# Kernel tuning notes

Hardware: AMD Instinct MI355X
Metric: run time of the kernel (lower is better)

## Reference

```python
import jax, jax.numpy as jnp
import numpy as np

# Tree / encoder dims (see shape_source): root + 4 middle + 16 leaves
T_DATA = 100000
T_V = 100
WIN = 2 * T_V - 1          # (T_V-1)*2 + 1 = 199, first MLP in_dim
HID = 256                  # hid_dim
N_MID = 4                  # numel(in_idx_list[0])  (middle-level latents)
N_LEAF = 16                # numel(out_idx_list[-1]) (leaf-level latents)


def setup_inputs() -> dict:
    key = jax.random.key(0)
    ks = jax.random.split(key, 6)
    sc = lambda k, shape, fan: jax.random.normal(k, shape, jnp.float32) * (1.0 / np.sqrt(fan))
    return {
        "V_in": jax.random.normal(ks[0], (T_DATA,), jnp.float32),
        "W1": sc(ks[1], (WIN, HID), WIN),
        "b1": jnp.zeros((HID,), jnp.float32),
        "W2": sc(ks[2], (HID, N_MID), HID),
        "b2": jnp.zeros((N_MID,), jnp.float32),
        # leaf_encoder = MLP(HID, HID, N_LEAF)
        "Wl1": sc(ks[3], (HID, HID), HID),
        "bl1": jnp.zeros((HID,), jnp.float32),
        "Wl2": sc(ks[4], (HID, N_LEAF), HID),
        "bl2": jnp.zeros((N_LEAF,), jnp.float32),
    }


def reference(V_in, W1, b1, W2, b2, Wl1, bl1, Wl2, bl2):
    """Vectorized LVAE_shGLM.Encoder: the original loops over every timestep t,
    slicing pad_V_in[t:t+2*T_V-1] and running MLP.encode chains per step.
    Here all T windows are processed as one batched GEMM chain.
    MLP.encode(x) = (h = relu(x@W1+b1), mu = h@W2+b2)."""
    T = V_in.shape[0]
    pad = jnp.zeros((T + 2 * (T_V - 1),), V_in.dtype).at[T_V - 1:T_V - 1 + T].set(V_in)
    idx = jnp.arange(T)[:, None] + jnp.arange(WIN)[None, :]
    windows = pad[idx]
    # middle encoder (level 0 of the dendritic tree)
    h_mid = jax.nn.relu(windows @ W1 + b1)          # [T, HID]
    mu_mid = h_mid @ W2 + b2                        # [T, N_MID]
    # leaf encoder consumes the middle hidden state
    h_leaf = jax.nn.relu(h_mid @ Wl1 + bl1)         # [T, HID]
    mu_leaf = h_leaf @ Wl2 + bl2                    # [T, N_LEAF]
    # up_mu_array[t] = [middle mus (count 0..N_MID), leaf mus (N_MID..sub_no-1)]
    return jnp.concatenate([mu_mid, mu_leaf], axis=1)  # [T, sub_no-1] = [T, 20]
```

## Files before the change

kernel.cpp:

```cpp
#include <hip/hip_runtime.h>


typedef __bf16 bf16;
typedef __bf16 bf16x8 __attribute__((ext_vector_type(8)));
typedef float  f32x4  __attribute__((ext_vector_type(4)));
typedef float  f32x16 __attribute__((ext_vector_type(16)));

constexpr int T_DATA = 100000;
constexpr int T_V    = 100;
constexpr int WIN    = 199;
constexpr int HID    = 256;
constexpr int BT     = 64;
constexpr int HSTR   = 264;
constexpr int VLEN   = 288;
constexpr int VSTR   = 296;

constexpr int PWL1_OFF = 104 * 512;
constexpr int PW2_OFF  = 232 * 512;
constexpr int PWL2_OFF = 240 * 512;

__global__ void pack_weights(const float* __restrict__ W1, const float* __restrict__ W2,
                             const float* __restrict__ Wl1, const float* __restrict__ Wl2,
                             bf16* __restrict__ ws) {
  const int gid  = blockIdx.x * blockDim.x + threadIdx.x;
  const int lane = gid & 63;
  const int grp  = gid >> 6;
  bf16x8 v;
  if (grp < 104) {
    const int kt = grp >> 3, nt = grp & 7, n = nt * 32 + (lane & 31);
#pragma unroll
    for (int j = 0; j < 8; ++j) {
      const int k = kt * 16 + (lane >> 5) * 8 + j;
      v[j] = (k < WIN) ? (bf16)W1[k * HID + n] : (bf16)0.0f;
    }
  } else if (grp < 232) {
    const int q = grp - 104;
    const int kt = q >> 3, nt = q & 7, n = nt * 32 + (lane & 31);
#pragma unroll
    for (int j = 0; j < 8; ++j) {
      const int k = kt * 16 + (lane >> 5) * 8 + j;
      v[j] = (bf16)Wl1[k * HID + n];
    }
  } else if (grp < 240) {
    const int kt = grp - 232, m = lane & 15;
#pragma unroll
    for (int j = 0; j < 8; ++j) {
      const int k = kt * 32 + (lane >> 4) * 8 + j;
      v[j] = (m < 4) ? (bf16)W2[k * 4 + m] : (bf16)0.0f;
    }
  } else {
    const int kt = grp - 240, m = lane & 15;
#pragma unroll
    for (int j = 0; j < 8; ++j) {
      const int k = kt * 32 + (lane >> 4) * 8 + j;
      v[j] = (bf16)Wl2[k * 16 + m];
    }
  }
  *reinterpret_cast<bf16x8*>(ws + (size_t)gid * 8) = v;
}

__global__ __launch_bounds__(512, 4) void fused_enc(
    const float* __restrict__ V, const float* __restrict__ b1,
    const float* __restrict__ b2, const float* __restrict__ bl1,
    const float* __restrict__ bl2, const bf16* __restrict__ ws,
    float* __restrict__ out) {
  __shared__ bf16 Vdup[8][VSTR];
  __shared__ bf16 hmid[BT * HSTR];
  __shared__ bf16 hleaf[BT * HSTR];

  const int tid  = threadIdx.x;
  const int lane = tid & 63;
  const int w    = tid >> 6;
  const int c5   = lane & 31;
  const int hi   = lane >> 5;
  const int m    = lane & 15;
  const int g    = lane >> 4;
  const long t0  = (long)blockIdx.x * BT;

  for (int c = tid; c < 8 * VLEN; c += 512) {
    const int p = c / VLEN, q = c - p * VLEN;
    const long src = t0 + q + p - (T_V - 1);
    const float v = (src >= 0 && src < T_DATA) ? V[src] : 0.0f;
    Vdup[p][q] = (bf16)v;
  }
  __syncthreads();

  const int p  = lane & 7;
  const int qb = (c5 + hi * 8) - p;
  const bf16* vrow = &Vdup[p][0];

  f32x16 acc0 = {}, acc1 = {};

#pragma unroll
  for (int kt = 0; kt < 13; ++kt) {
    const bf16x8 b  = *reinterpret_cast<const bf16x8*>(
        ws + (size_t)(kt * 8 + w) * 512 + lane * 8);
    const bf16x8 a0 = *reinterpret_cast<const bf16x8*>(vrow + qb + kt * 16);
    const bf16x8 a1 = *reinterpret_cast<const bf16x8*>(vrow + qb + kt * 16 + 32);
    acc0 = __builtin_amdgcn_mfma_f32_32x32x16_bf16(a0, b, acc0, 0, 0, 0);
    acc1 = __builtin_amdgcn_mfma_f32_32x32x16_bf16(a1, b, acc1, 0, 0, 0);
  }

  const int   col = w * 32 + c5;
  const float bb1 = b1[col];
#pragma unroll
  for (int r = 0; r < 16; ++r) {
    const int row = (r & 3) + 8 * (r >> 2) + 4 * hi;
    hmid[row * HSTR + col]        = (bf16)fmaxf(acc0[r] + bb1, 0.0f);
    hmid[(row + 32) * HSTR + col] = (bf16)fmaxf(acc1[r] + bb1, 0.0f);
  }
  __syncthreads();

  acc0 = (f32x16){};
  acc1 = (f32x16){};
#pragma unroll
  for (int kt = 0; kt < 16; ++kt) {
    const bf16x8 b  = *reinterpret_cast<const bf16x8*>(
        ws + PWL1_OFF + (size_t)(kt * 8 + w) * 512 + lane * 8);
    const int koff = kt * 16 + hi * 8;
    const bf16x8 a0 = *reinterpret_cast<const bf16x8*>(&hmid[c5 * HSTR + koff]);
    const bf16x8 a1 = *reinterpret_cast<const bf16x8*>(&hmid[(32 + c5) * HSTR + koff]);
    acc0 = __builtin_amdgcn_mfma_f32_32x32x16_bf16(a0, b, acc0, 0, 0, 0);
    acc1 = __builtin_amdgcn_mfma_f32_32x32x16_bf16(a1, b, acc1, 0, 0, 0);
  }

  const float bbl = bl1[col];
#pragma unroll
  for (int r = 0; r < 16; ++r) {
    const int row = (r & 3) + 8 * (r >> 2) + 4 * hi;
    hleaf[row * HSTR + col]        = (bf16)fmaxf(acc0[r] + bbl, 0.0f);
    hleaf[(row + 32) * HSTR + col] = (bf16)fmaxf(acc1[r] + bbl, 0.0f);
  }
  __syncthreads();

  const bf16* hb   = (w < 4) ? hmid : hleaf;
  const bf16* bwp  = ws + ((w < 4) ? PW2_OFF : PWL2_OFF);
  const int   wr   = w & 3;
  f32x4 mu = {0.f, 0.f, 0.f, 0.f};
#pragma unroll
  for (int kt = 0; kt < 8; ++kt) {
    const bf16x8 a = *reinterpret_cast<const bf16x8*>(
        &hb[(wr * 16 + m) * HSTR + kt * 32 + g * 8]);
    const bf16x8 b = *reinterpret_cast<const bf16x8*>(bwp + (size_t)kt * 512 + lane * 8);
    mu = __builtin_amdgcn_mfma_f32_16x16x32_bf16(a, b, mu, 0, 0, 0);
  }

  if (w < 4) {
    const float b2v = (m < 4) ? b2[m] : 0.0f;
#pragma unroll
    for (int j = 0; j < 4; ++j) {
      const long t = t0 + wr * 16 + g * 4 + j;
      if (t < T_DATA && m < 4) out[t * 20 + m] = mu[j] + b2v;
    }
  } else {
    const float blv = bl2[m];
#pragma unroll
    for (int j = 0; j < 4; ++j) {
      const long t = t0 + wr * 16 + g * 4 + j;
      if (t < T_DATA) out[t * 20 + 4 + m] = mu[j] + blv;
    }
  }
}

extern "C" void kernel_launch(void* const* d_in, const int* in_sizes, int n_in,
                              void* d_out, int out_size, void* d_ws, size_t ws_size,
                              hipStream_t stream) {
  const float* V   = (const float*)d_in[0];
  const float* W1  = (const float*)d_in[1];
  const float* b1  = (const float*)d_in[2];
  const float* W2  = (const float*)d_in[3];
  const float* b2  = (const float*)d_in[4];
  const float* Wl1 = (const float*)d_in[5];
  const float* bl1 = (const float*)d_in[6];
  const float* Wl2 = (const float*)d_in[7];
  const float* bl2 = (const float*)d_in[8];
  bf16* ws = (bf16*)d_ws;
  float* out = (float*)d_out;

  pack_weights<<<62, 256, 0, stream>>>(W1, W2, Wl1, Wl2, ws);

  const int grid = (T_DATA + BT - 1) / BT;
  fused_enc<<<grid, 512, 0, stream>>>(V, b1, b2, bl1, bl2, ws, out);
}
```

Measured before the change: 43.76 us.

## Double row tile to 128 and reuse one shared buffer for both hidden layers

Result: faster. 42.75 us (-2.3%).

```diff
diff --git a/kernel.cpp b/kernel.cpp
--- a/kernel.cpp
+++ b/kernel.cpp
@@ -10,10 +10,10 @@
 constexpr int T_V    = 100;
 constexpr int WIN    = 199;
 constexpr int HID    = 256;
-constexpr int BT     = 64;
+constexpr int BT     = 128;
 constexpr int HSTR   = 264;
-constexpr int VLEN   = 288;
-constexpr int VSTR   = 296;
+constexpr int VLEN   = 352;
+constexpr int VSTR   = 360;
 
 constexpr int PWL1_OFF = 104 * 512;
 constexpr int PW2_OFF  = 232 * 512;
@@ -65,8 +65,7 @@
     const float* __restrict__ bl2, const bf16* __restrict__ ws,
     float* __restrict__ out) {
   __shared__ bf16 Vdup[8][VSTR];
-  __shared__ bf16 hmid[BT * HSTR];
-  __shared__ bf16 hleaf[BT * HSTR];
+  __shared__ bf16 hbuf[BT * HSTR];
 
   const int tid  = threadIdx.x;
   const int lane = tid & 63;
@@ -89,74 +88,89 @@
   const int qb = (c5 + hi * 8) - p;
   const bf16* vrow = &Vdup[p][0];
 
-  f32x16 acc0 = {}, acc1 = {};
+  f32x16 acc[4];
+#pragma unroll
+  for (int rt = 0; rt < 4; ++rt) acc[rt] = (f32x16){};
 
 #pragma unroll
   for (int kt = 0; kt < 13; ++kt) {
-    const bf16x8 b  = *reinterpret_cast<const bf16x8*>(
+    const bf16x8 b = *reinterpret_cast<const bf16x8*>(
         ws + (size_t)(kt * 8 + w) * 512 + lane * 8);
-    const bf16x8 a0 = *reinterpret_cast<const bf16x8*>(vrow + qb + kt * 16);
-    const bf16x8 a1 = *reinterpret_cast<const bf16x8*>(vrow + qb + kt * 16 + 32);
-    acc0 = __builtin_amdgcn_mfma_f32_32x32x16_bf16(a0, b, acc0, 0, 0, 0);
-    acc1 = __builtin_amdgcn_mfma_f32_32x32x16_bf16(a1, b, acc1, 0, 0, 0);
+#pragma unroll
+    for (int rt = 0; rt < 4; ++rt) {
+      const bf16x8 a = *reinterpret_cast<const bf16x8*>(vrow + qb + kt * 16 + rt * 32);
+      acc[rt] = __builtin_amdgcn_mfma_f32_32x32x16_bf16(a, b, acc[rt], 0, 0, 0);
+    }
   }
 
   const int   col = w * 32 + c5;
   const float bb1 = b1[col];
 #pragma unroll
-  for (int r = 0; r < 16; ++r) {
-    const int row = (r & 3) + 8 * (r >> 2) + 4 * hi;
-    hmid[row * HSTR + col]        = (bf16)fmaxf(acc0[r] + bb1, 0.0f);
-    hmid[(row + 32) * HSTR + col] = (bf16)fmaxf(acc1[r] + bb1, 0.0f);
-  }
+  for (int rt = 0; rt < 4; ++rt)
+#pragma unroll
+    for (int r = 0; r < 16; ++r) {
+      const int row = rt * 32 + (r & 3) + 8 * (r >> 2) + 4 * hi;
+      hbuf[row * HSTR + col] = (bf16)fmaxf(acc[rt][r] + bb1, 0.0f);
+    }
   __syncthreads();
 
-  acc0 = (f32x16){};
-  acc1 = (f32x16){};
+#pragma unroll
+  for (int rt = 0; rt < 4; ++rt) acc[rt] = (f32x16){};
 #pragma unroll
   for (int kt = 0; kt < 16; ++kt) {
-    const bf16x8 b  = *reinterpret_cast<const bf16x8*>(
+    const bf16x8 b = *reinterpret_cast<const bf16x8*>(
         ws + PWL1_OFF + (size_t)(kt * 8 + w) * 512 + lane * 8);
     const int koff = kt * 16 + hi * 8;
-    const bf16x8 a0 = *reinterpret_cast<const bf16x8*>(&hmid[c5 * HSTR + koff]);
-    const bf16x8 a1 = *reinterpret_cast<const bf16x8*>(&hmid[(32 + c5) * HSTR + koff]);
-    acc0 = __builtin_amdgcn_mfma_f32_32x32x16_bf16(a0, b, acc0, 0, 0, 0);
-    acc1 = __builtin_amdgcn_mfma_f32_32x32x16_bf16(a1, b, acc1, 0, 0, 0);
+#pragma unroll
+    for (int rt = 0; rt < 4; ++rt) {
+      const bf16x8 a = *reinterpret_cast<const bf16x8*>(&hbuf[(rt * 32 + c5) * HSTR + koff]);
+      acc[rt] = __builtin_amdgcn_mfma_f32_32x32x16_bf16(a, b, acc[rt], 0, 0, 0);
+    }
   }
 
-  const float bbl = bl1[col];
-#pragma unroll
-  for (int r = 0; r < 16; ++r) {
-    const int row = (r & 3) + 8 * (r >> 2) + 4 * hi;
-    hleaf[row * HSTR + col]        = (bf16)fmaxf(acc0[r] + bbl, 0.0f);
-    hleaf[(row + 32) * HSTR + col] = (bf16)fmaxf(acc1[r] + bbl, 0.0f);
-  }
-  __syncthreads();
-
-  const bf16* hb   = (w < 4) ? hmid : hleaf;
-  const bf16* bwp  = ws + ((w < 4) ? PW2_OFF : PWL2_OFF);
-  const int   wr   = w & 3;
   f32x4 mu = {0.f, 0.f, 0.f, 0.f};
 #pragma unroll
   for (int kt = 0; kt < 8; ++kt) {
     const bf16x8 a = *reinterpret_cast<const bf16x8*>(
-        &hb[(wr * 16 + m) * HSTR + kt * 32 + g * 8]);
-    const bf16x8 b = *reinterpret_cast<const bf16x8*>(bwp + (size_t)kt * 512 + lane * 8);
+        &hbuf[(w * 16 + m) * HSTR + kt * 32 + g * 8]);
+    const bf16x8 b = *reinterpret_cast<const bf16x8*>(
+        ws + PW2_OFF + (size_t)kt * 512 + lane * 8);
     mu = __builtin_amdgcn_mfma_f32_16x16x32_bf16(a, b, mu, 0, 0, 0);
   }
-
-  if (w < 4) {
+  {
     const float b2v = (m < 4) ? b2[m] : 0.0f;
 #pragma unroll
     for (int j = 0; j < 4; ++j) {
-      const long t = t0 + wr * 16 + g * 4 + j;
+      const long t = t0 + w * 16 + g * 4 + j;
       if (t < T_DATA && m < 4) out[t * 20 + m] = mu[j] + b2v;
     }
-  } else {
+  }
+  __syncthreads();
+
+  const float bbl = bl1[col];
+#pragma unroll
+  for (int rt = 0; rt < 4; ++rt)
+#pragma unroll
+    for (int r = 0; r < 16; ++r) {
+      const int row = rt * 32 + (r & 3) + 8 * (r >> 2) + 4 * hi;
+      hbuf[row * HSTR + col] = (bf16)fmaxf(acc[rt][r] + bbl, 0.0f);
+    }
+  __syncthreads();
+
+  mu = (f32x4){0.f, 0.f, 0.f, 0.f};
+#pragma unroll
+  for (int kq = 0; kq < 8; ++kq) {
+    const bf16x8 a = *reinterpret_cast<const bf16x8*>(
+        &hbuf[(w * 16 + m) * HSTR + kq * 32 + g * 8]);
+    const bf16x8 b = *reinterpret_cast<const bf16x8*>(
+        ws + PWL2_OFF + (size_t)kq * 512 + lane * 8);
+    mu = __builtin_amdgcn_mfma_f32_16x16x32_bf16(a, b, mu, 0, 0, 0);
+  }
+  {
     const float blv = bl2[m];
 #pragma unroll
     for (int j = 0; j < 4; ++j) {
-      const long t = t0 + wr * 16 + g * 4 + j;
+      const long t = t0 + w * 16 + g * 4 + j;
       if (t < T_DATA) out[t * 20 + 4 + m] = mu[j] + blv;
     }
   }
```

## Reuse one shared hidden buffer for mid and leaf activations to raise occupancy

Applied to the files above, without the earlier changes.

After: 45.68 us. +4.4%, slower.

```diff
diff --git a/kernel.cpp b/kernel.cpp
--- a/kernel.cpp
+++ b/kernel.cpp
@@ -59,18 +59,18 @@
   *reinterpret_cast<bf16x8*>(ws + (size_t)gid * 8) = v;
 }
 
-__global__ __launch_bounds__(512, 4) void fused_enc(
+__global__ __launch_bounds__(512, 6) void fused_enc(
     const float* __restrict__ V, const float* __restrict__ b1,
     const float* __restrict__ b2, const float* __restrict__ bl1,
     const float* __restrict__ bl2, const bf16* __restrict__ ws,
     float* __restrict__ out) {
   __shared__ bf16 Vdup[8][VSTR];
-  __shared__ bf16 hmid[BT * HSTR];
-  __shared__ bf16 hleaf[BT * HSTR];
+  __shared__ bf16 hbuf[BT * HSTR];
 
   const int tid  = threadIdx.x;
   const int lane = tid & 63;
   const int w    = tid >> 6;
+  const int wr   = w & 3;
   const int c5   = lane & 31;
   const int hi   = lane >> 5;
   const int m    = lane & 15;
@@ -106,8 +106,8 @@
 #pragma unroll
   for (int r = 0; r < 16; ++r) {
     const int row = (r & 3) + 8 * (r >> 2) + 4 * hi;
-    hmid[row * HSTR + col]        = (bf16)fmaxf(acc0[r] + bb1, 0.0f);
-    hmid[(row + 32) * HSTR + col] = (bf16)fmaxf(acc1[r] + bb1, 0.0f);
+    hbuf[row * HSTR + col]        = (bf16)fmaxf(acc0[r] + bb1, 0.0f);
+    hbuf[(row + 32) * HSTR + col] = (bf16)fmaxf(acc1[r] + bb1, 0.0f);
   }
   __syncthreads();
 
@@ -115,49 +115,58 @@
   acc1 = (f32x16){};
 #pragma unroll
   for (int kt = 0; kt < 16; ++kt) {
-    const bf16x8 b  = *reinterpret_cast<const bf16x8*>(
+    const bf16x8 b = *reinterpret_cast<const bf16x8*>(
         ws + PWL1_OFF + (size_t)(kt * 8 + w) * 512 + lane * 8);
     const int koff = kt * 16 + hi * 8;
-    const bf16x8 a0 = *reinterpret_cast<const bf16x8*>(&hmid[c5 * HSTR + koff]);
-    const bf16x8 a1 = *reinterpret_cast<const bf16x8*>(&hmid[(32 + c5) * HSTR + koff]);
+    const bf16x8 a0 = *reinterpret_cast<const bf16x8*>(&hbuf[c5 * HSTR + koff]);
+    const bf16x8 a1 = *reinterpret_cast<const bf16x8*>(&hbuf[(32 + c5) * HSTR + koff]);
     acc0 = __builtin_amdgcn_mfma_f32_32x32x16_bf16(a0, b, acc0, 0, 0, 0);
     acc1 = __builtin_amdgcn_mfma_f32_32x32x16_bf16(a1, b, acc1, 0, 0, 0);
   }
+
+  f32x4 mu = {0.f, 0.f, 0.f, 0.f};
+#pragma unroll
+  for (int kt = 0; kt < 8; ++kt) {
+    const bf16x8 a = *reinterpret_cast<const bf16x8*>(
+        &hbuf[(wr * 16 + m) * HSTR + kt * 32 + g * 8]);
+    const bf16x8 b = *reinterpret_cast<const bf16x8*>(
+        ws + PW2_OFF + (size_t)kt * 512 + lane * 8);
+    mu = __builtin_amdgcn_mfma_f32_16x16x32_bf16(a, b, mu, 0, 0, 0);
+  }
+  {
+    const float b2v = (m < 4) ? b2[m] : 0.0f;
+#pragma unroll
+    for (int j = 0; j < 4; ++j) {
+      const long t = t0 + wr * 16 + g * 4 + j;
+      if (t < T_DATA && w < 4 && m < 4) out[t * 20 + m] = mu[j] + b2v;
+    }
+  }
+  __syncthreads();
 
   const float bbl = bl1[col];
 #pragma unroll
   for (int r = 0; r < 16; ++r) {
     const int row = (r & 3) + 8 * (r >> 2) + 4 * hi;
-    hleaf[row * HSTR + col]        = (bf16)fmaxf(acc0[r] + bbl, 0.0f);
-    hleaf[(row + 32) * HSTR + col] = (bf16)fmaxf(acc1[r] + bbl, 0.0f);
+    hbuf[row * HSTR + col]        = (bf16)fmaxf(acc0[r] + bbl, 0.0f);
+    hbuf[(row + 32) * HSTR + col] = (bf16)fmaxf(acc1[r] + bbl, 0.0f);
   }
   __syncthreads();
 
-  const bf16* hb   = (w < 4) ? hmid : hleaf;
-  const bf16* bwp  = ws + ((w < 4) ? PW2_OFF : PWL2_OFF);
-  const int   wr   = w & 3;
-  f32x4 mu = {0.f, 0.f, 0.f, 0.f};
+  mu = (f32x4){0.f, 0.f, 0.f, 0.f};
 #pragma unroll
-  for (int kt = 0; kt < 8; ++kt) {
+  for (int kq = 0; kq < 8; ++kq) {
     const bf16x8 a = *reinterpret_cast<const bf16x8*>(
-        &hb[(wr * 16 + m) * HSTR + kt * 32 + g * 8]);
-    const bf16x8 b = *reinterpret_cast<const bf16x8*>(bwp + (size_t)kt * 512 + lane * 8);
+        &hbuf[(wr * 16 + m) * HSTR + kq * 32 + g * 8]);
+    const bf16x8 b = *reinterpret_cast<const bf16x8*>(
+        ws + PWL2_OFF + (size_t)kq * 512 + lane * 8);
     mu = __builtin_amdgcn_mfma_f32_16x16x32_bf16(a, b, mu, 0, 0, 0);
   }
-
-  if (w < 4) {
-    const float b2v = (m < 4) ? b2[m] : 0.0f;
-#pragma unroll
-    for (int j = 0; j < 4; ++j) {
-      const long t = t0 + wr * 16 + g * 4 + j;
-      if (t < T_DATA && m < 4) out[t * 20 + m] = mu[j] + b2v;
-    }
-  } else {
+  {
     const float blv = bl2[m];
 #pragma unroll
     for (int j = 0; j < 4; ++j) {
       const long t = t0 + wr * 16 + g * 4 + j;
-      if (t < T_DATA) out[t * 20 + 4 + m] = mu[j] + blv;
+      if (t < T_DATA && w >= 4) out[t * 20 + 4 + m] = mu[j] + blv;
     }
   }
 }
```
